# Performance work log

Measured on AMD Instinct MI355X. Metric: run time of the kernel, lower is better.

## Reference

```python
import jax, jax.numpy as jnp
import numpy as np

B, T, D = 128, 512, 400
N_VALS, N_ACTS = 1024, 128

def setup_inputs() -> dict:
    key = jax.random.key(0)
    ks = jax.random.split(key, 7)
    H_utt = jax.random.normal(ks[0], (B, T, D), dtype=jnp.float32)
    c_utt = jax.random.normal(ks[1], (B, D), dtype=jnp.float32)
    C_acts = jax.random.normal(ks[2], (B, N_ACTS, D), dtype=jnp.float32)
    C_vals = jax.random.normal(ks[3], (N_VALS, 1, D), dtype=jnp.float32)
    W_score = jax.random.normal(ks[4], (1, D), dtype=jnp.float32) * (1.0 / np.sqrt(D))
    b_score = jnp.zeros((1,), dtype=jnp.float32)
    lens = jax.random.randint(ks[5], (B,), T // 2, T + 1, dtype=jnp.int64 if jax.config.read('jax_enable_x64') else jnp.int32)
    lens = lens.at[0].set(T)  # ensure max(lens) == T so masking matches torch semantics
    return {"H_utt": H_utt, "c_utt": c_utt, "C_acts": C_acts, "C_vals": C_vals,
            "W_score": W_score, "b_score": b_score, "utterance_len": lens}

def reference(H_utt, c_utt, C_acts, C_vals, W_score, b_score, utterance_len):
    vals = C_vals[:, 0, :]                                   # [V, D]
    # --- y_utts: default attention of each value vector over utterance states ---
    scores = jnp.einsum('btd,vd->bvt', H_utt, vals)          # mul+sum scoring
    mask = jnp.arange(T)[None, :] < utterance_len[:, None]   # [B, T]
    scores = jnp.where(mask[:, None, :], scores, -jnp.inf)
    probs = jax.nn.softmax(scores, axis=-1)                  # [B, V, T]
    q_utts = jnp.einsum('bvt,btd->bvd', probs, H_utt)        # weighted sum contexts
    y_utts = jnp.einsum('bvd,d->bv', q_utts, W_score[0]) + b_score[0]  # utt_scorer
    # --- y_acts: attention of c_utt over per-example act vectors, then score vs vals ---
    s2 = jnp.einsum('bad,bd->ba', C_acts, c_utt)
    p2 = jax.nn.softmax(s2, axis=-1)
    q_acts = jnp.einsum('ba,bad->bd', p2, C_acts)            # [B, D]
    y_acts = q_acts @ vals.T                                 # [B, V]
    return (y_utts, y_acts)
```

## Files before the change

### kernel.cpp

```cpp
#include <hip/hip_runtime.h>
#include <hip/hip_bf16.h>

#define B_  128
#define T_  512
#define D_  400
#define NV  1024
#define NA  128

#define LDH  424
#define NT   64
#define MV   128

typedef __bf16 bf16_t;
typedef bf16_t bf16x8 __attribute__((ext_vector_type(8)));
typedef bf16_t bf16x4 __attribute__((ext_vector_type(4)));
typedef float  floatx4 __attribute__((ext_vector_type(4)));

__device__ inline void async_copy16(const void* g, void* l) {
    __builtin_amdgcn_global_load_lds(
        (const __attribute__((address_space(1))) unsigned int*)g,
        (__attribute__((address_space(3))) unsigned int*)l, 16, 0, 0);
}

__device__ inline float dot4(float4 a, float4 b) {
    return a.x * b.x + a.y * b.y + a.z * b.z + a.w * b.w;
}

__global__ __launch_bounds__(256) void hw_prep_kernel(const float* __restrict__ H,
                                                      const float* __restrict__ W,
                                                      float* __restrict__ hw,
                                                      bf16_t* __restrict__ Hbf) {
    int wave = threadIdx.x >> 6;
    int lane = threadIdx.x & 63;
    long row = (long)blockIdx.x * 4 + wave;
    const float* h = H + row * D_;
    bf16_t* orow = Hbf + row * (long)LDH;
    float acc = 0.f;
    if (lane < 50) {
        const float4* p  = (const float4*)(h + lane * 8);
        const float4* wp = (const float4*)(W + lane * 8);
        float4 x = p[0], y = p[1];
        float4 wx = wp[0], wy = wp[1];
        acc = dot4(x, wx) + dot4(y, wy);
        bf16x8 f;
        f[0] = (bf16_t)x.x; f[1] = (bf16_t)x.y; f[2] = (bf16_t)x.z; f[3] = (bf16_t)x.w;
        f[4] = (bf16_t)y.x; f[5] = (bf16_t)y.y; f[6] = (bf16_t)y.z; f[7] = (bf16_t)y.w;
        *(bf16x8*)(orow + lane * 8) = f;
    } else if (lane < 53) {
        bf16x8 z;
#pragma unroll
        for (int j = 0; j < 8; ++j) z[j] = (bf16_t)0.0f;
        *(bf16x8*)(orow + 400 + (lane - 50) * 8) = z;
    }
#pragma unroll
    for (int off = 1; off < 64; off <<= 1) acc += __shfl_xor(acc, off, 64);
    if (lane == 0) hw[row] = acc;
}

__global__ __launch_bounds__(256) void hw_kernel(const float* __restrict__ H,
                                                 const float* __restrict__ W,
                                                 float* __restrict__ hw) {
    int wave = threadIdx.x >> 6;
    int lane = threadIdx.x & 63;
    long row = (long)blockIdx.x * 4 + wave;
    const float* h = H + row * D_;
    float acc = 0.f;
    for (int k = lane; k < D_; k += 64) acc += h[k] * W[k];
#pragma unroll
    for (int off = 1; off < 64; off <<= 1) acc += __shfl_xor(acc, off, 64);
    if (lane == 0) hw[row] = acc;
}

__global__ __launch_bounds__(256) void s2_kernel(const float* __restrict__ Ca,
                                                 const float* __restrict__ cu,
                                                 float* __restrict__ s2) {
    int wave = threadIdx.x >> 6;
    int lane = threadIdx.x & 63;
    long row = (long)blockIdx.x * 4 + wave;
    int b = (int)(row >> 7);
    const float4* a4 = (const float4*)(Ca + row * (long)D_);
    const float4* c4 = (const float4*)(cu + (long)b * D_);
    float acc = dot4(a4[lane], c4[lane]);
    if (lane < 36) acc += dot4(a4[lane + 64], c4[lane + 64]);
#pragma unroll
    for (int off = 1; off < 64; off <<= 1) acc += __shfl_xor(acc, off, 64);
    if (lane == 0) s2[row] = acc;
}

__global__ __launch_bounds__(256) void qacts_kernel(const float* __restrict__ s2,
                                                    const float* __restrict__ Ca,
                                                    float* __restrict__ q_ws) {
    __shared__ float p_lds[NA];
    __shared__ float red[8];
    __shared__ __align__(16) float4 part[100];
    int b = blockIdx.x;
    int tid = threadIdx.x, wave = tid >> 6, lane = tid & 63;

    float s = (tid < NA) ? s2[(long)b * NA + tid] : -3.0e38f;
    float m = s;
#pragma unroll
    for (int off = 1; off < 64; off <<= 1) m = fmaxf(m, __shfl_xor(m, off, 64));
    if (lane == 0) red[wave] = m;
    __syncthreads();
    m = fmaxf(red[0], red[1]);
    float e = (tid < NA) ? __expf(s - m) : 0.f;
    float sum = e;
#pragma unroll
    for (int off = 1; off < 64; off <<= 1) sum += __shfl_xor(sum, off, 64);
    if (lane == 0) red[4 + wave] = sum;
    __syncthreads();
    float S = red[4] + red[5];
    if (tid < NA) p_lds[tid] = e / S;
    __syncthreads();

    int c4 = tid % 100;
    int half = tid / 100;
    float4 acc0 = {0.f, 0.f, 0.f, 0.f};
    if (tid < 200) {
        const float4* Cb4 = (const float4*)(Ca + (size_t)b * NA * D_);
        float4 acc1 = {0.f, 0.f, 0.f, 0.f};
        int a0 = half * 64;
#pragma unroll 4
        for (int a = 0; a < 64; a += 2) {
            float p0 = p_lds[a0 + a], p1 = p_lds[a0 + a + 1];
            float4 x0 = Cb4[(size_t)(a0 + a) * 100 + c4];
            float4 x1 = Cb4[(size_t)(a0 + a + 1) * 100 + c4];
            acc0.x += p0 * x0.x; acc0.y += p0 * x0.y; acc0.z += p0 * x0.z; acc0.w += p0 * x0.w;
            acc1.x += p1 * x1.x; acc1.y += p1 * x1.y; acc1.z += p1 * x1.z; acc1.w += p1 * x1.w;
        }
        acc0.x += acc1.x; acc0.y += acc1.y; acc0.z += acc1.z; acc0.w += acc1.w;
        if (half == 1) part[c4] = acc0;
    }
    __syncthreads();
    if (tid < 100) {
        float4 o = part[c4];
        o.x += acc0.x; o.y += acc0.y; o.z += acc0.z; o.w += acc0.w;
        ((float4*)(q_ws + (size_t)b * D_))[c4] = o;
    }
}

__global__ __launch_bounds__(256) void yacts_kernel(const float* __restrict__ q_ws,
                                                    const float* __restrict__ Cv,
                                                    float* __restrict__ out) {
    int wave = threadIdx.x >> 6;
    int lane = threadIdx.x & 63;
    long grp = (long)blockIdx.x * 4 + wave;
    int b = (int)(grp >> 8);
    int v0 = (int)(grp & 255) * 4;
    const float4* q4 = (const float4*)(q_ws + (size_t)b * D_);
    float4 qa = q4[lane];
    float4 qb = (lane < 36) ? q4[lane + 64] : make_float4(0.f, 0.f, 0.f, 0.f);
    float acc[4];
#pragma unroll
    for (int r = 0; r < 4; ++r) {
        const float4* v4 = (const float4*)(Cv + (size_t)(v0 + r) * D_);
        float4 x = v4[lane];
        acc[r] = dot4(x, qa);
        if (lane < 36) acc[r] += dot4(v4[lane + 64], qb);
    }
#pragma unroll
    for (int off = 1; off < 64; off <<= 1) {
#pragma unroll
        for (int r = 0; r < 4; ++r) acc[r] += __shfl_xor(acc[r], off, 64);
    }
    if (lane == 0) {
        float4 o = make_float4(acc[0], acc[1], acc[2], acc[3]);
        *(float4*)(out + (size_t)B_ * NV + (size_t)b * NV + v0) = o;
    }
}

template<int PRE>
__global__ __launch_bounds__(256, 2) void main_kernel(const float* __restrict__ H,
                                                      const bf16_t* __restrict__ Hbf,
                                                      const float* __restrict__ Cv,
                                                      const float* __restrict__ hw,
                                                      const float* __restrict__ bs,
                                                      const int* __restrict__ lens,
                                                      float* __restrict__ out) {
    __shared__ bf16_t h_lds[NT * LDH];
    __shared__ float hw_lds[NT];

    int i = blockIdx.x;
    int xcd = i & 7, vc = (i >> 3) & 7, bb = i >> 6;
    int b = xcd + 8 * bb;
    int vbase = vc * MV;

    int tid = threadIdx.x;
    int wave = tid >> 6, lane = tid & 63;
    int lrow = lane & 15, quad = lane >> 4;

    int len = lens[b];
    float b0 = bs[0];

    if (!PRE) {
        for (int idx = tid; idx < NT * (LDH - D_); idx += 256) {
            int r = idx / (LDH - D_), c = idx % (LDH - D_);
            h_lds[r * LDH + D_ + c] = (bf16_t)0.0f;
        }
    }

    bf16x8 afrag[2][13];
#pragma unroll
    for (int set = 0; set < 2; ++set) {
        const float* vrow = Cv + (size_t)(vbase + wave * 32 + set * 16 + lrow) * D_;
#pragma unroll
        for (int kk = 0; kk < 13; ++kk) {
            int k0 = kk * 32 + quad * 8;
            bf16x8 f;
            if (k0 >= D_) {
#pragma unroll
                for (int j = 0; j < 8; ++j) f[j] = (bf16_t)0.0f;
            } else {
                const float4* p = (const float4*)(vrow + k0);
                float4 x = p[0], y = p[1];
                f[0] = (bf16_t)x.x; f[1] = (bf16_t)x.y;
                f[2] = (bf16_t)x.z; f[3] = (bf16_t)x.w;
                f[4] = (bf16_t)y.x; f[5] = (bf16_t)y.y;
                f[6] = (bf16_t)y.z; f[7] = (bf16_t)y.w;
            }
            afrag[set][kk] = f;
        }
    }

    float m_s[2][4], l_s[2][4], a_s[2][4];
#pragma unroll
    for (int set = 0; set < 2; ++set)
#pragma unroll
        for (int r = 0; r < 4; ++r) { m_s[set][r] = -3.0e38f; l_s[set][r] = 0.f; a_s[set][r] = 0.f; }

    int ntiles = (len + NT - 1) / NT;
    const float* Hb = H + (size_t)b * T_ * D_;
    const bf16_t* Hbfb = Hbf + (size_t)b * T_ * LDH;

    for (int tt = 0; tt < ntiles; ++tt) {
        int t0 = tt * NT;
        __syncthreads();
        if (PRE) {
            const char* gt = (const char*)(Hbfb + (size_t)t0 * LDH);
            char* lt = (char*)h_lds;
#pragma unroll 1
            for (int c = wave; c < 53; c += 4)
                async_copy16(gt + c * 1024 + lane * 16, lt + c * 1024 + lane * 16);
        } else {
            for (int idx = tid; idx < NT * (D_ / 4); idx += 256) {
                int r = idx / (D_ / 4), c4 = idx % (D_ / 4);
                float4 x = *(const float4*)(Hb + (size_t)(t0 + r) * D_ + c4 * 4);
                bf16x4 f;
                f[0] = (bf16_t)x.x; f[1] = (bf16_t)x.y;
                f[2] = (bf16_t)x.z; f[3] = (bf16_t)x.w;
                *(bf16x4*)(&h_lds[r * LDH + c4 * 4]) = f;
            }
        }
        if (tid < NT) hw_lds[tid] = hw[(size_t)b * T_ + t0 + tid];
        __syncthreads();

        floatx4 c[2][4];
        floatx4 zero4 = {0.f, 0.f, 0.f, 0.f};
#pragma unroll
        for (int set = 0; set < 2; ++set)
#pragma unroll
            for (int s = 0; s < 4; ++s) c[set][s] = zero4;

#pragma unroll
        for (int kk = 0; kk < 13; ++kk) {
            int koff = kk * 32 + quad * 8;
#pragma unroll
            for (int s = 0; s < 4; ++s) {
                bf16x8 bfr = *(const bf16x8*)(&h_lds[(s * 16 + lrow) * LDH + koff]);
                c[0][s] = __builtin_amdgcn_mfma_f32_16x16x32_bf16(afrag[0][kk], bfr, c[0][s], 0, 0, 0);
                c[1][s] = __builtin_amdgcn_mfma_f32_16x16x32_bf16(afrag[1][kk], bfr, c[1][s], 0, 0, 0);
            }
        }

        if (t0 + NT > len) {
#pragma unroll
            for (int s = 0; s < 4; ++s) {
                int t = t0 + s * 16 + lrow;
                if (t >= len) {
#pragma unroll
                    for (int set = 0; set < 2; ++set) {
                        c[set][s][0] = -3.0e38f; c[set][s][1] = -3.0e38f;
                        c[set][s][2] = -3.0e38f; c[set][s][3] = -3.0e38f;
                    }
                }
            }
        }

        float hwv[4];
#pragma unroll
        for (int s = 0; s < 4; ++s) hwv[s] = hw_lds[s * 16 + lrow];

#pragma unroll
        for (int set = 0; set < 2; ++set)
#pragma unroll
            for (int r = 0; r < 4; ++r) {
                float cm = fmaxf(fmaxf(c[set][0][r], c[set][1][r]),
                                 fmaxf(c[set][2][r], c[set][3][r]));
                float mn = fmaxf(m_s[set][r], cm);
                float alpha = __expf(m_s[set][r] - mn);
                float ps = 0.f, qs = 0.f;
#pragma unroll
                for (int s = 0; s < 4; ++s) {
                    float p = __expf(c[set][s][r] - mn);
                    ps += p;
                    qs += p * hwv[s];
                }
                l_s[set][r] = l_s[set][r] * alpha + ps;
                a_s[set][r] = a_s[set][r] * alpha + qs;
                m_s[set][r] = mn;
            }
    }

#pragma unroll
    for (int set = 0; set < 2; ++set)
#pragma unroll
        for (int r = 0; r < 4; ++r) {
            float m = m_s[set][r], l = l_s[set][r], a = a_s[set][r];
#pragma unroll
            for (int off = 1; off < 16; off <<= 1) {
                float mo = __shfl_xor(m, off, 64);
                float lo = __shfl_xor(l, off, 64);
                float ao = __shfl_xor(a, off, 64);
                float mn = fmaxf(m, mo);
                float f1 = __expf(m - mn), f2 = __expf(mo - mn);
                l = l * f1 + lo * f2;
                a = a * f1 + ao * f2;
                m = mn;
            }
            if (lrow == 0) {
                int v = vbase + wave * 32 + set * 16 + quad * 4 + r;
                out[(size_t)b * NV + v] = a / l + b0;
            }
        }
}

extern "C" void kernel_launch(void* const* d_in, const int* in_sizes, int n_in,
                              void* d_out, int out_size, void* d_ws, size_t ws_size,
                              hipStream_t stream) {
    const float* H    = (const float*)d_in[0];
    const float* cu   = (const float*)d_in[1];
    const float* Ca   = (const float*)d_in[2];
    const float* Cv   = (const float*)d_in[3];
    const float* W    = (const float*)d_in[4];
    const float* bs   = (const float*)d_in[5];
    const int*   lens = (const int*)d_in[6];
    float* out = (float*)d_out;

    float*  hw   = (float*)d_ws;
    float*  q_ws = hw + (size_t)B_ * T_;
    float*  s2   = q_ws + (size_t)B_ * D_;
    bf16_t* Hbf  = (bf16_t*)(s2 + (size_t)B_ * NA);

    size_t need = ((size_t)B_ * T_ + (size_t)B_ * D_ + (size_t)B_ * NA) * sizeof(float)
                + (size_t)B_ * T_ * LDH * sizeof(bf16_t);
    bool pre = (ws_size >= need);

    if (pre) {
        hw_prep_kernel<<<dim3(B_ * T_ / 4), dim3(256), 0, stream>>>(H, W, hw, Hbf);
    } else {
        hw_kernel<<<dim3(B_ * T_ / 4), dim3(256), 0, stream>>>(H, W, hw);
    }
    s2_kernel<<<dim3(B_ * NA / 4), dim3(256), 0, stream>>>(Ca, cu, s2);
    qacts_kernel<<<dim3(B_), dim3(256), 0, stream>>>(s2, Ca, q_ws);
    if (pre) {
        main_kernel<1><<<dim3(1024), dim3(256), 0, stream>>>(H, Hbf, Cv, hw, bs, lens, out);
    } else {
        main_kernel<0><<<dim3(1024), dim3(256), 0, stream>>>(H, Hbf, Cv, hw, bs, lens, out);
    }
    yacts_kernel<<<dim3(B_ * NV / 16), dim3(256), 0, stream>>>(q_ws, Cv, out);
}
```

Measured before the change: 279.5 us.

## Fuse prep and s2 launches, fold yacts into main kernel, halve time tile

Merges the hw/bf16 prep and s2 score kernels into one launch, and appends the y_acts dot-product blocks to the main attention grid so one launch is dropped. The main kernel's time tile shrinks from 64 to 32 rows with a 3-blocks-per-CU occupancy hint, which cuts LDS use. The online softmax now keeps one shared running max per lane instead of eight, which removes exp work. Risks are more tile iterations with more barriers, register pressure under the tighter launch bound, and the shared max making scaling less precise for rows with very different ranges.

```diff
diff --git a/kernel.cpp b/kernel.cpp
--- a/kernel.cpp
+++ b/kernel.cpp
@@ -8,8 +8,9 @@
 #define NA  128
 
 #define LDH  424
-#define NT   64
+#define NT   32
 #define MV   128
+#define MAIN_BLOCKS 1024
 
 typedef __bf16 bf16_t;
 typedef bf16_t bf16x8 __attribute__((ext_vector_type(8)));
@@ -26,65 +27,78 @@
     return a.x * b.x + a.y * b.y + a.z * b.z + a.w * b.w;
 }
 
-__global__ __launch_bounds__(256) void hw_prep_kernel(const float* __restrict__ H,
-                                                      const float* __restrict__ W,
-                                                      float* __restrict__ hw,
-                                                      bf16_t* __restrict__ Hbf) {
+__global__ __launch_bounds__(256) void prep_kernel(const float* __restrict__ H,
+                                                   const float* __restrict__ W,
+                                                   const float* __restrict__ Ca,
+                                                   const float* __restrict__ cu,
+                                                   float* __restrict__ hw,
+                                                   bf16_t* __restrict__ Hbf,
+                                                   float* __restrict__ s2) {
     int wave = threadIdx.x >> 6;
     int lane = threadIdx.x & 63;
-    long row = (long)blockIdx.x * 4 + wave;
-    const float* h = H + row * D_;
-    bf16_t* orow = Hbf + row * (long)LDH;
-    float acc = 0.f;
-    if (lane < 50) {
-        const float4* p  = (const float4*)(h + lane * 8);
-        const float4* wp = (const float4*)(W + lane * 8);
-        float4 x = p[0], y = p[1];
-        float4 wx = wp[0], wy = wp[1];
-        acc = dot4(x, wx) + dot4(y, wy);
-        bf16x8 f;
-        f[0] = (bf16_t)x.x; f[1] = (bf16_t)x.y; f[2] = (bf16_t)x.z; f[3] = (bf16_t)x.w;
-        f[4] = (bf16_t)y.x; f[5] = (bf16_t)y.y; f[6] = (bf16_t)y.z; f[7] = (bf16_t)y.w;
-        *(bf16x8*)(orow + lane * 8) = f;
-    } else if (lane < 53) {
-        bf16x8 z;
-#pragma unroll
-        for (int j = 0; j < 8; ++j) z[j] = (bf16_t)0.0f;
-        *(bf16x8*)(orow + 400 + (lane - 50) * 8) = z;
-    }
-#pragma unroll
-    for (int off = 1; off < 64; off <<= 1) acc += __shfl_xor(acc, off, 64);
-    if (lane == 0) hw[row] = acc;
-}
-
-__global__ __launch_bounds__(256) void hw_kernel(const float* __restrict__ H,
-                                                 const float* __restrict__ W,
-                                                 float* __restrict__ hw) {
+    if (blockIdx.x < B_ * T_ / 4) {
+        long row = (long)blockIdx.x * 4 + wave;
+        const float* h = H + row * D_;
+        bf16_t* orow = Hbf + row * (long)LDH;
+        float acc = 0.f;
+        if (lane < 50) {
+            const float4* p  = (const float4*)(h + lane * 8);
+            const float4* wp = (const float4*)(W + lane * 8);
+            float4 x = p[0], y = p[1];
+            acc = dot4(x, wp[0]) + dot4(y, wp[1]);
+            bf16x8 f;
+            f[0] = (bf16_t)x.x; f[1] = (bf16_t)x.y; f[2] = (bf16_t)x.z; f[3] = (bf16_t)x.w;
+            f[4] = (bf16_t)y.x; f[5] = (bf16_t)y.y; f[6] = (bf16_t)y.z; f[7] = (bf16_t)y.w;
+            *(bf16x8*)(orow + lane * 8) = f;
+        } else if (lane < 53) {
+            bf16x8 z;
+#pragma unroll
+            for (int j = 0; j < 8; ++j) z[j] = (bf16_t)0.0f;
+            *(bf16x8*)(orow + 400 + (lane - 50) * 8) = z;
+        }
+#pragma unroll
+        for (int off = 1; off < 64; off <<= 1) acc += __shfl_xor(acc, off, 64);
+        if (lane == 0) hw[row] = acc;
+    } else {
+        long row = (long)(blockIdx.x - B_ * T_ / 4) * 4 + wave;
+        int b = (int)(row >> 7);
+        const float4* a4 = (const float4*)(Ca + row * (long)D_);
+        const float4* c4 = (const float4*)(cu + (long)b * D_);
+        float acc = dot4(a4[lane], c4[lane]);
+        if (lane < 36) acc += dot4(a4[lane + 64], c4[lane + 64]);
+#pragma unroll
+        for (int off = 1; off < 64; off <<= 1) acc += __shfl_xor(acc, off, 64);
+        if (lane == 0) s2[row] = acc;
+    }
+}
+
+__global__ __launch_bounds__(256) void prep_nb_kernel(const float* __restrict__ H,
+                                                      const float* __restrict__ W,
+                                                      const float* __restrict__ Ca,
+                                                      const float* __restrict__ cu,
+                                                      float* __restrict__ hw,
+                                                      float* __restrict__ s2) {
     int wave = threadIdx.x >> 6;
     int lane = threadIdx.x & 63;
-    long row = (long)blockIdx.x * 4 + wave;
-    const float* h = H + row * D_;
-    float acc = 0.f;
-    for (int k = lane; k < D_; k += 64) acc += h[k] * W[k];
-#pragma unroll
-    for (int off = 1; off < 64; off <<= 1) acc += __shfl_xor(acc, off, 64);
-    if (lane == 0) hw[row] = acc;
-}
-
-__global__ __launch_bounds__(256) void s2_kernel(const float* __restrict__ Ca,
-                                                 const float* __restrict__ cu,
-                                                 float* __restrict__ s2) {
-    int wave = threadIdx.x >> 6;
-    int lane = threadIdx.x & 63;
-    long row = (long)blockIdx.x * 4 + wave;
-    int b = (int)(row >> 7);
-    const float4* a4 = (const float4*)(Ca + row * (long)D_);
-    const float4* c4 = (const float4*)(cu + (long)b * D_);
-    float acc = dot4(a4[lane], c4[lane]);
-    if (lane < 36) acc += dot4(a4[lane + 64], c4[lane + 64]);
-#pragma unroll
-    for (int off = 1; off < 64; off <<= 1) acc += __shfl_xor(acc, off, 64);
-    if (lane == 0) s2[row] = acc;
+    if (blockIdx.x < B_ * T_ / 4) {
+        long row = (long)blockIdx.x * 4 + wave;
+        const float* h = H + row * D_;
+        float acc = 0.f;
+        for (int k = lane; k < D_; k += 64) acc += h[k] * W[k];
+#pragma unroll
+        for (int off = 1; off < 64; off <<= 1) acc += __shfl_xor(acc, off, 64);
+        if (lane == 0) hw[row] = acc;
+    } else {
+        long row = (long)(blockIdx.x - B_ * T_ / 4) * 4 + wave;
+        int b = (int)(row >> 7);
+        const float4* a4 = (const float4*)(Ca + row * (long)D_);
+        const float4* c4 = (const float4*)(cu + (long)b * D_);
+        float acc = dot4(a4[lane], c4[lane]);
+        if (lane < 36) acc += dot4(a4[lane + 64], c4[lane + 64]);
+#pragma unroll
+        for (int off = 1; off < 64; off <<= 1) acc += __shfl_xor(acc, off, 64);
+        if (lane == 0) s2[row] = acc;
+    }
 }
 
 __global__ __launch_bounds__(256) void qacts_kernel(const float* __restrict__ s2,
@@ -139,56 +153,53 @@
     }
 }
 
-__global__ __launch_bounds__(256) void yacts_kernel(const float* __restrict__ q_ws,
-                                                    const float* __restrict__ Cv,
-                                                    float* __restrict__ out) {
-    int wave = threadIdx.x >> 6;
-    int lane = threadIdx.x & 63;
-    long grp = (long)blockIdx.x * 4 + wave;
-    int b = (int)(grp >> 8);
-    int v0 = (int)(grp & 255) * 4;
-    const float4* q4 = (const float4*)(q_ws + (size_t)b * D_);
-    float4 qa = q4[lane];
-    float4 qb = (lane < 36) ? q4[lane + 64] : make_float4(0.f, 0.f, 0.f, 0.f);
-    float acc[4];
-#pragma unroll
-    for (int r = 0; r < 4; ++r) {
-        const float4* v4 = (const float4*)(Cv + (size_t)(v0 + r) * D_);
-        float4 x = v4[lane];
-        acc[r] = dot4(x, qa);
-        if (lane < 36) acc[r] += dot4(v4[lane + 64], qb);
-    }
-#pragma unroll
-    for (int off = 1; off < 64; off <<= 1) {
-#pragma unroll
-        for (int r = 0; r < 4; ++r) acc[r] += __shfl_xor(acc[r], off, 64);
-    }
-    if (lane == 0) {
-        float4 o = make_float4(acc[0], acc[1], acc[2], acc[3]);
-        *(float4*)(out + (size_t)B_ * NV + (size_t)b * NV + v0) = o;
-    }
-}
-
 template<int PRE>
-__global__ __launch_bounds__(256, 2) void main_kernel(const float* __restrict__ H,
+__global__ __launch_bounds__(256, 3) void main_kernel(const float* __restrict__ H,
                                                       const bf16_t* __restrict__ Hbf,
                                                       const float* __restrict__ Cv,
                                                       const float* __restrict__ hw,
                                                       const float* __restrict__ bs,
                                                       const int* __restrict__ lens,
+                                                      const float* __restrict__ q_ws,
                                                       float* __restrict__ out) {
-    __shared__ bf16_t h_lds[NT * LDH];
+    __shared__ bf16_t h_lds[NT * LDH + 256];
     __shared__ float hw_lds[NT];
+
+    int tid = threadIdx.x;
+    int wave = tid >> 6, lane = tid & 63;
+
+    if (blockIdx.x >= MAIN_BLOCKS) {
+        long grp = (long)(blockIdx.x - MAIN_BLOCKS) * 4 + wave;
+        int b = (int)(grp >> 8);
+        int v0 = (int)(grp & 255) * 4;
+        const float4* q4 = (const float4*)(q_ws + (size_t)b * D_);
+        float4 qa = q4[lane];
+        float4 qb = (lane < 36) ? q4[lane + 64] : make_float4(0.f, 0.f, 0.f, 0.f);
+        float acc[4];
+#pragma unroll
+        for (int r = 0; r < 4; ++r) {
+            const float4* v4 = (const float4*)(Cv + (size_t)(v0 + r) * D_);
+            acc[r] = dot4(v4[lane], qa);
+            if (lane < 36) acc[r] += dot4(v4[lane + 64], qb);
+        }
+#pragma unroll
+        for (int off = 1; off < 64; off <<= 1) {
+#pragma unroll
+            for (int r = 0; r < 4; ++r) acc[r] += __shfl_xor(acc[r], off, 64);
+        }
+        if (lane == 0) {
+            float4 o = make_float4(acc[0], acc[1], acc[2], acc[3]);
+            *(float4*)(out + (size_t)B_ * NV + (size_t)b * NV + v0) = o;
+        }
+        return;
+    }
 
     int i = blockIdx.x;
     int xcd = i & 7, vc = (i >> 3) & 7, bb = i >> 6;
     int b = xcd + 8 * bb;
     int vbase = vc * MV;
 
-    int tid = threadIdx.x;
-    int wave = tid >> 6, lane = tid & 63;
     int lrow = lane & 15, quad = lane >> 4;
-
     int len = lens[b];
     float b0 = bs[0];
 
@@ -222,11 +233,12 @@
         }
     }
 
-    float m_s[2][4], l_s[2][4], a_s[2][4];
+    float m_s = -3.0e38f;
+    float l_s[2][4], a_s[2][4];
 #pragma unroll
     for (int set = 0; set < 2; ++set)
 #pragma unroll
-        for (int r = 0; r < 4; ++r) { m_s[set][r] = -3.0e38f; l_s[set][r] = 0.f; a_s[set][r] = 0.f; }
+        for (int r = 0; r < 4; ++r) { l_s[set][r] = 0.f; a_s[set][r] = 0.f; }
 
     int ntiles = (len + NT - 1) / NT;
     const float* Hb = H + (size_t)b * T_ * D_;
@@ -239,7 +251,7 @@
             const char* gt = (const char*)(Hbfb + (size_t)t0 * LDH);
             char* lt = (char*)h_lds;
 #pragma unroll 1
-            for (int c = wave; c < 53; c += 4)
+            for (int c = wave; c < 27; c += 4)
                 async_copy16(gt + c * 1024 + lane * 16, lt + c * 1024 + lane * 16);
         } else {
             for (int idx = tid; idx < NT * (D_ / 4); idx += 256) {
@@ -254,18 +266,18 @@
         if (tid < NT) hw_lds[tid] = hw[(size_t)b * T_ + t0 + tid];
         __syncthreads();
 
-        floatx4 c[2][4];
+        floatx4 c[2][2];
         floatx4 zero4 = {0.f, 0.f, 0.f, 0.f};
 #pragma unroll
         for (int set = 0; set < 2; ++set)
 #pragma unroll
-            for (int s = 0; s < 4; ++s) c[set][s] = zero4;
+            for (int s = 0; s < 2; ++s) c[set][s] = zero4;
 
 #pragma unroll
         for (int kk = 0; kk < 13; ++kk) {
             int koff = kk * 32 + quad * 8;
 #pragma unroll
-            for (int s = 0; s < 4; ++s) {
+            for (int s = 0; s < 2; ++s) {
                 bf16x8 bfr = *(const bf16x8*)(&h_lds[(s * 16 + lrow) * LDH + koff]);
                 c[0][s] = __builtin_amdgcn_mfma_f32_16x16x32_bf16(afrag[0][kk], bfr, c[0][s], 0, 0, 0);
                 c[1][s] = __builtin_amdgcn_mfma_f32_16x16x32_bf16(afrag[1][kk], bfr, c[1][s], 0, 0, 0);
@@ -274,7 +286,7 @@
 
         if (t0 + NT > len) {
 #pragma unroll
-            for (int s = 0; s < 4; ++s) {
+            for (int s = 0; s < 2; ++s) {
                 int t = t0 + s * 16 + lrow;
                 if (t >= len) {
 #pragma unroll
@@ -286,28 +298,24 @@
             }
         }
 
-        float hwv[4];
-#pragma unroll
-        for (int s = 0; s < 4; ++s) hwv[s] = hw_lds[s * 16 + lrow];
-
+        float hw0 = hw_lds[lrow], hw1 = hw_lds[16 + lrow];
+
+        float cm = fmaxf(fmaxf(fmaxf(c[0][0][0], c[0][0][1]), fmaxf(c[0][0][2], c[0][0][3])),
+                         fmaxf(fmaxf(c[0][1][0], c[0][1][1]), fmaxf(c[0][1][2], c[0][1][3])));
+        cm = fmaxf(cm,
+             fmaxf(fmaxf(fmaxf(c[1][0][0], c[1][0][1]), fmaxf(c[1][0][2], c[1][0][3])),
+                   fmaxf(fmaxf(c[1][1][0], c[1][1][1]), fmaxf(c[1][1][2], c[1][1][3]))));
+        float mn = fmaxf(m_s, cm);
+        float alpha = __expf(m_s - mn);
+        m_s = mn;
 #pragma unroll
         for (int set = 0; set < 2; ++set)
 #pragma unroll
             for (int r = 0; r < 4; ++r) {
-                float cm = fmaxf(fmaxf(c[set][0][r], c[set][1][r]),
-                                 fmaxf(c[set][2][r], c[set][3][r]));
-                float mn = fmaxf(m_s[set][r], cm);
-                float alpha = __expf(m_s[set][r] - mn);
-                float ps = 0.f, qs = 0.f;
-#pragma unroll
-                for (int s = 0; s < 4; ++s) {
-                    float p = __expf(c[set][s][r] - mn);
-                    ps += p;
-                    qs += p * hwv[s];
-                }
-                l_s[set][r] = l_s[set][r] * alpha + ps;
-                a_s[set][r] = a_s[set][r] * alpha + qs;
-                m_s[set][r] = mn;
+                float p0 = __expf(c[set][0][r] - mn);
+                float p1 = __expf(c[set][1][r] - mn);
+                l_s[set][r] = l_s[set][r] * alpha + (p0 + p1);
+                a_s[set][r] = a_s[set][r] * alpha + (p0 * hw0 + p1 * hw1);
             }
     }
 
@@ -315,17 +323,17 @@
     for (int set = 0; set < 2; ++set)
 #pragma unroll
         for (int r = 0; r < 4; ++r) {
-            float m = m_s[set][r], l = l_s[set][r], a = a_s[set][r];
+            float m = m_s, l = l_s[set][r], a = a_s[set][r];
 #pragma unroll
             for (int off = 1; off < 16; off <<= 1) {
                 float mo = __shfl_xor(m, off, 64);
                 float lo = __shfl_xor(l, off, 64);
                 float ao = __shfl_xor(a, off, 64);
-                float mn = fmaxf(m, mo);
-                float f1 = __expf(m - mn), f2 = __expf(mo - mn);
+                float mx = fmaxf(m, mo);
+                float f1 = __expf(m - mx), f2 = __expf(mo - mx);
                 l = l * f1 + lo * f2;
                 a = a * f1 + ao * f2;
-                m = mn;
+                m = mx;
             }
             if (lrow == 0) {
                 int v = vbase + wave * 32 + set * 16 + quad * 4 + r;
@@ -352,20 +360,21 @@
     bf16_t* Hbf  = (bf16_t*)(s2 + (size_t)B_ * NA);
 
     size_t need = ((size_t)B_ * T_ + (size_t)B_ * D_ + (size_t)B_ * NA) * sizeof(float)
-                + (size_t)B_ * T_ * LDH * sizeof(bf16_t);
+                + (size_t)B_ * T_ * LDH * sizeof(bf16_t)
+                + 4096;
     bool pre = (ws_size >= need);
 
+    int prep_blocks = B_ * T_ / 4 + B_ * NA / 4;
     if (pre) {
-        hw_prep_kernel<<<dim3(B_ * T_ / 4), dim3(256), 0, stream>>>(H, W, hw, Hbf);
+        prep_kernel<<<dim3(prep_blocks), dim3(256), 0, stream>>>(H, W, Ca, cu, hw, Hbf, s2);
     } else {
-        hw_kernel<<<dim3(B_ * T_ / 4), dim3(256), 0, stream>>>(H, W, hw);
-    }
-    s2_kernel<<<dim3(B_ * NA / 4), dim3(256), 0, stream>>>(Ca, cu, s2);
+        prep_nb_kernel<<<dim3(prep_blocks), dim3(256), 0, stream>>>(H, W, Ca, cu, hw, s2);
+    }
     qacts_kernel<<<dim3(B_), dim3(256), 0, stream>>>(s2, Ca, q_ws);
+    int fused_blocks = MAIN_BLOCKS + B_ * NV / 16;
     if (pre) {
-        main_kernel<1><<<dim3(1024), dim3(256), 0, stream>>>(H, Hbf, Cv, hw, bs, lens, out);
+        main_kernel<1><<<dim3(fused_blocks), dim3(256), 0, stream>>>(H, Hbf, Cv, hw, bs, lens, q_ws, out);
     } else {
-        main_kernel<0><<<dim3(1024), dim3(256), 0, stream>>>(H, Hbf, Cv, hw, bs, lens, out);
-    }
-    yacts_kernel<<<dim3(B_ * NV / 16), dim3(256), 0, stream>>>(q_ws, Cv, out);
-}
+        main_kernel<0><<<dim3(fused_blocks), dim3(256), 0, stream>>>(H, Hbf, Cv, hw, bs, lens, q_ws, out);
+    }
+}
```

Measured after the change: 288.5 us. +3.2%, slower.
